# Optimization experiments

Measured on AMD Instinct MI355X. Metric: run time of the kernel, lower is better.

## Reference

```python
import jax, jax.numpy as jnp
import numpy as np


def setup_inputs() -> dict:
    key = jax.random.key(0)
    kq, kk, kv = jax.random.split(key, 3)
    B, L, S, H, E = 2, 2048, 2048, 16, 64
    queries = jax.random.normal(kq, (B, L, H, E), dtype=jnp.float32)
    keys = jax.random.normal(kk, (B, S, H, E), dtype=jnp.float32)
    values = jax.random.normal(kv, (B, S, H, E), dtype=jnp.float32)
    # TriangularCausalMask: True strictly above the diagonal (positions to mask)
    causal = jnp.triu(jnp.ones((L, S), dtype=jnp.bool_), k=1)
    attn_mask = jnp.broadcast_to(causal[None, None, :, :], (B, 1, L, S))
    return {"queries": queries, "keys": keys, "values": values, "attn_mask": attn_mask}


def reference(queries, keys, values, attn_mask):
    # queries: [B,L,H,E], keys/values: [B,S,H,E], attn_mask: [B,1,L,S] bool
    E = queries.shape[-1]
    scale = 1.0 / jnp.sqrt(jnp.asarray(E, dtype=queries.dtype))
    scores = jnp.einsum('blhe,bshe->bhls', queries, keys)      # [B,H,L,S]
    scores = jnp.where(attn_mask, -jnp.inf, scores)
    A = jax.nn.softmax(scale * scores, axis=-1)                # dropout is identity in eval
    V = jnp.einsum('bhls,bshd->blhd', A, values)               # [B,L,H,D]
    return V, A
```

## Files before the change

kernel.cpp:

```cpp
#include <hip/hip_runtime.h>
#include <hip/hip_bf16.h>


#define B_ 2
#define L_ 2048
#define S_ 2048
#define H_ 16
#define E_ 64
#define HE 1024
#define KP 72
#define PP 68

typedef __attribute__((ext_vector_type(8))) __bf16 bfrag;
typedef __attribute__((ext_vector_type(4))) float f32x4;

__device__ __forceinline__ unsigned short f2bu(float x) {
    __bf16 b = (__bf16)x;
    return __builtin_bit_cast(unsigned short, b);
}

__global__ __launch_bounds__(256, 2)
void fullattn_kernel(const float* __restrict__ Qg,
                     const float* __restrict__ Kg,
                     const float* __restrict__ Vg,
                     float* __restrict__ Vout,
                     float* __restrict__ Aout)
{
    __shared__ __align__(16) __bf16 Ks[64 * KP];
    __shared__ __align__(16) __bf16 Vt[64 * KP];
    __shared__ __align__(16) float  Pw[4][16 * PP];

    const int tid  = threadIdx.x;
    const int wave = tid >> 6;
    const int lane = tid & 63;
    const int ln   = lane & 15;
    const int quad = lane >> 4;
    const int lq   = quad * 4;

    const int qt = blockIdx.x;
    const int bh = blockIdx.y;
    const int b  = bh >> 4;
    const int h  = bh & 15;

    const int q0  = qt * 64;
    const int q0w = q0 + wave * 16;

    const float* qbase = Qg + ((size_t)b * L_ * H_ + h) * E_;
    const float* kbase = Kg + ((size_t)b * S_ * H_ + h) * E_;
    const float* vbase = Vg + ((size_t)b * S_ * H_ + h) * E_;
    float* arow0 = Aout + (size_t)bh * L_ * S_;

    bfrag qf[2];
    {
        const float* qr = qbase + (size_t)(q0w + ln) * HE;
        #pragma unroll
        for (int kc = 0; kc < 2; ++kc) {
            const float* p = qr + kc * 32 + quad * 8;
            float4 a0 = *(const float4*)(p);
            float4 a1 = *(const float4*)(p + 4);
            bfrag f;
            f[0] = (__bf16)(a0.x * 0.125f); f[1] = (__bf16)(a0.y * 0.125f);
            f[2] = (__bf16)(a0.z * 0.125f); f[3] = (__bf16)(a0.w * 0.125f);
            f[4] = (__bf16)(a1.x * 0.125f); f[5] = (__bf16)(a1.y * 0.125f);
            f[6] = (__bf16)(a1.z * 0.125f); f[7] = (__bf16)(a1.w * 0.125f);
            qf[kc] = f;
        }
    }

    const int r  = tid >> 2;
    const int c0 = tid & 3;

    float lsum[4] = {0.f, 0.f, 0.f, 0.f};
    for (int st = 0; st <= qt; ++st) {
        const int s0 = st * 64;
        __syncthreads();
        {
            const float* kr = kbase + (size_t)(s0 + r) * HE;
            #pragma unroll
            for (int i = 0; i < 4; ++i) {
                int f4 = c0 + i * 4;
                float4 kv = *(const float4*)(kr + f4 * 4);
                ushort4 kb;
                kb.x = f2bu(kv.x); kb.y = f2bu(kv.y);
                kb.z = f2bu(kv.z); kb.w = f2bu(kv.w);
                *(ushort4*)&Ks[r * KP + f4 * 4] = kb;
            }
        }
        __syncthreads();
        #pragma unroll
        for (int nc = 0; nc < 4; ++nc) {
            f32x4 acc = {0.f, 0.f, 0.f, 0.f};
            #pragma unroll
            for (int kc = 0; kc < 2; ++kc) {
                bfrag bk = *(const bfrag*)&Ks[(nc * 16 + ln) * KP + kc * 32 + quad * 8];
                acc = __builtin_amdgcn_mfma_f32_16x16x32_bf16(qf[kc], bk, acc, 0, 0, 0);
            }
            const int s_abs = s0 + nc * 16 + ln;
            #pragma unroll
            for (int rg = 0; rg < 4; ++rg) {
                const int q_abs = q0w + lq + rg;
                float e = (s_abs <= q_abs) ? __expf(acc[rg]) : 0.0f;
                lsum[rg] += e;
            }
        }
    }

    float inv_l[4];
    #pragma unroll
    for (int rg = 0; rg < 4; ++rg) {
        float v = lsum[rg];
        v += __shfl_xor(v, 1);
        v += __shfl_xor(v, 2);
        v += __shfl_xor(v, 4);
        v += __shfl_xor(v, 8);
        inv_l[rg] = 1.0f / v;
    }

    f32x4 oacc[4];
    #pragma unroll
    for (int dc = 0; dc < 4; ++dc) {
        f32x4 z = {0.f, 0.f, 0.f, 0.f};
        oacc[dc] = z;
    }

    const int wr = lane >> 2;
    const int wc = (lane & 3) * 4;

    for (int st = 0; st <= qt; ++st) {
        const int s0 = st * 64;
        __syncthreads();
        {
            const float* kr = kbase + (size_t)(s0 + r) * HE;
            const float* vr = vbase + (size_t)(s0 + r) * HE;
            #pragma unroll
            for (int i = 0; i < 4; ++i) {
                int f4 = c0 + i * 4;
                float4 kv = *(const float4*)(kr + f4 * 4);
                float4 vv = *(const float4*)(vr + f4 * 4);
                ushort4 kb;
                kb.x = f2bu(kv.x); kb.y = f2bu(kv.y);
                kb.z = f2bu(kv.z); kb.w = f2bu(kv.w);
                *(ushort4*)&Ks[r * KP + f4 * 4] = kb;
                const int d0 = f4 * 4;
                Vt[(d0 + 0) * KP + r] = (__bf16)vv.x;
                Vt[(d0 + 1) * KP + r] = (__bf16)vv.y;
                Vt[(d0 + 2) * KP + r] = (__bf16)vv.z;
                Vt[(d0 + 3) * KP + r] = (__bf16)vv.w;
            }
        }
        __syncthreads();

        #pragma unroll
        for (int nc = 0; nc < 4; ++nc) {
            f32x4 acc = {0.f, 0.f, 0.f, 0.f};
            #pragma unroll
            for (int kc = 0; kc < 2; ++kc) {
                bfrag bk = *(const bfrag*)&Ks[(nc * 16 + ln) * KP + kc * 32 + quad * 8];
                acc = __builtin_amdgcn_mfma_f32_16x16x32_bf16(qf[kc], bk, acc, 0, 0, 0);
            }
            const int s_abs = s0 + nc * 16 + ln;
            #pragma unroll
            for (int rg = 0; rg < 4; ++rg) {
                const int q_abs = q0w + lq + rg;
                float e = (s_abs <= q_abs) ? __expf(acc[rg]) : 0.0f;
                Pw[wave][(lq + rg) * PP + nc * 16 + ln] = e * inv_l[rg];
            }
        }

        bfrag af[2];
        #pragma unroll
        for (int kc = 0; kc < 2; ++kc) {
            const float* pp = &Pw[wave][ln * PP + kc * 32 + quad * 8];
            float4 p0 = *(const float4*)pp;
            float4 p1 = *(const float4*)(pp + 4);
            bfrag f;
            f[0] = (__bf16)p0.x; f[1] = (__bf16)p0.y;
            f[2] = (__bf16)p0.z; f[3] = (__bf16)p0.w;
            f[4] = (__bf16)p1.x; f[5] = (__bf16)p1.y;
            f[6] = (__bf16)p1.z; f[7] = (__bf16)p1.w;
            af[kc] = f;
        }

        #pragma unroll
        for (int dc = 0; dc < 4; ++dc) {
            #pragma unroll
            for (int kc = 0; kc < 2; ++kc) {
                bfrag bv = *(const bfrag*)&Vt[(dc * 16 + ln) * KP + kc * 32 + quad * 8];
                oacc[dc] = __builtin_amdgcn_mfma_f32_16x16x32_bf16(af[kc], bv, oacc[dc], 0, 0, 0);
            }
        }

        float* ar = arow0 + (size_t)(q0w + wr) * S_ + s0;
        #pragma unroll
        for (int c4 = 0; c4 < 4; ++c4) {
            float4 v4 = *(const float4*)&Pw[wave][wr * PP + wc + c4 * 16];
            *(float4*)(ar + wc + c4 * 16) = v4;
        }
    }

    {
        const float4 z4 = {0.f, 0.f, 0.f, 0.f};
        for (int st = qt + 1; st < S_ / 64; ++st) {
            float* ar = arow0 + (size_t)(q0w + wr) * S_ + st * 64;
            #pragma unroll
            for (int c4 = 0; c4 < 4; ++c4)
                *(float4*)(ar + wc + c4 * 16) = z4;
        }
    }

    #pragma unroll
    for (int rg = 0; rg < 4; ++rg) {
        float* vr = Vout + ((size_t)(b * L_ + q0w + lq + rg) * H_ + h) * E_;
        #pragma unroll
        for (int dc = 0; dc < 4; ++dc)
            vr[dc * 16 + ln] = oacc[dc][rg];
    }
}

extern "C" void kernel_launch(void* const* d_in, const int* in_sizes, int n_in,
                              void* d_out, int out_size, void* d_ws, size_t ws_size,
                              hipStream_t stream) {
    const float* Q = (const float*)d_in[0];
    const float* K = (const float*)d_in[1];
    const float* V = (const float*)d_in[2];
    float* out  = (float*)d_out;
    float* Vo   = out;
    float* Ao   = out + (size_t)B_ * L_ * H_ * E_;
    dim3 grid(L_ / 64, B_ * H_);
    fullattn_kernel<<<grid, 256, 0, stream>>>(Q, K, V, Vo, Ao);
}
```

Baseline: 728.7 us.

## Prefetch K/V tiles into registers, balance causal tiles, raise occupancy, set MFMA priority

Loads the next K (and V) tile into registers while the current tile is converted and consumed, so global-load latency overlaps with compute. Block-to-query-tile mapping is interleaved so short and long causal rows are paired, which evens out the load across CUs. Launch bounds are raised to 4 blocks per CU and s_setprio is set around the MFMA sections. The risks are extra register pressure from the prefetch buffers under the tighter occupancy bound, and possible spills.

After: 725.8 us. About the same (-0.4%).

```diff
diff --git a/kernel.cpp b/kernel.cpp
--- a/kernel.cpp
+++ b/kernel.cpp
@@ -19,7 +19,7 @@
     return __builtin_bit_cast(unsigned short, b);
 }
 
-__global__ __launch_bounds__(256, 2)
+__global__ __launch_bounds__(256, 4)
 void fullattn_kernel(const float* __restrict__ Qg,
                      const float* __restrict__ Kg,
                      const float* __restrict__ Vg,
@@ -37,7 +37,8 @@
     const int quad = lane >> 4;
     const int lq   = quad * 4;
 
-    const int qt = blockIdx.x;
+    const int bx = blockIdx.x;
+    const int qt = (bx & 1) ? (31 - (bx >> 1)) : (bx >> 1);
     const int bh = blockIdx.y;
     const int b  = bh >> 4;
     const int h  = bh & 15;
@@ -71,37 +72,60 @@
     const int c0 = tid & 3;
 
     float lsum[4] = {0.f, 0.f, 0.f, 0.f};
+
+    float4 kpre[4];
+    {
+        const float* kr = kbase + (size_t)r * HE;
+        #pragma unroll
+        for (int i = 0; i < 4; ++i)
+            kpre[i] = *(const float4*)(kr + (c0 + i * 4) * 4);
+    }
+
     for (int st = 0; st <= qt; ++st) {
-        const int s0 = st * 64;
-        __syncthreads();
-        {
-            const float* kr = kbase + (size_t)(s0 + r) * HE;
-            #pragma unroll
-            for (int i = 0; i < 4; ++i) {
-                int f4 = c0 + i * 4;
-                float4 kv = *(const float4*)(kr + f4 * 4);
-                ushort4 kb;
-                kb.x = f2bu(kv.x); kb.y = f2bu(kv.y);
-                kb.z = f2bu(kv.z); kb.w = f2bu(kv.w);
-                *(ushort4*)&Ks[r * KP + f4 * 4] = kb;
-            }
+        __syncthreads();
+        #pragma unroll
+        for (int i = 0; i < 4; ++i) {
+            int f4 = c0 + i * 4;
+            ushort4 kb;
+            kb.x = f2bu(kpre[i].x); kb.y = f2bu(kpre[i].y);
+            kb.z = f2bu(kpre[i].z); kb.w = f2bu(kpre[i].w);
+            *(ushort4*)&Ks[r * KP + f4 * 4] = kb;
+        }
+        if (st < qt) {
+            const float* kr = kbase + (size_t)((st + 1) * 64 + r) * HE;
+            #pragma unroll
+            for (int i = 0; i < 4; ++i)
+                kpre[i] = *(const float4*)(kr + (c0 + i * 4) * 4);
         }
         __syncthreads();
         #pragma unroll
         for (int nc = 0; nc < 4; ++nc) {
             f32x4 acc = {0.f, 0.f, 0.f, 0.f};
+            __builtin_amdgcn_s_setprio(1);
             #pragma unroll
             for (int kc = 0; kc < 2; ++kc) {
                 bfrag bk = *(const bfrag*)&Ks[(nc * 16 + ln) * KP + kc * 32 + quad * 8];
                 acc = __builtin_amdgcn_mfma_f32_16x16x32_bf16(qf[kc], bk, acc, 0, 0, 0);
             }
-            const int s_abs = s0 + nc * 16 + ln;
+            __builtin_amdgcn_s_setprio(0);
+            const int s_abs = st * 64 + nc * 16 + ln;
             #pragma unroll
             for (int rg = 0; rg < 4; ++rg) {
                 const int q_abs = q0w + lq + rg;
                 float e = (s_abs <= q_abs) ? __expf(acc[rg]) : 0.0f;
                 lsum[rg] += e;
             }
+        }
+    }
+
+    float4 kp2[4], vp2[4];
+    {
+        const float* kr = kbase + (size_t)r * HE;
+        const float* vr = vbase + (size_t)r * HE;
+        #pragma unroll
+        for (int i = 0; i < 4; ++i) {
+            kp2[i] = *(const float4*)(kr + (c0 + i * 4) * 4);
+            vp2[i] = *(const float4*)(vr + (c0 + i * 4) * 4);
         }
     }
 
@@ -127,25 +151,27 @@
     const int wc = (lane & 3) * 4;
 
     for (int st = 0; st <= qt; ++st) {
-        const int s0 = st * 64;
-        __syncthreads();
-        {
-            const float* kr = kbase + (size_t)(s0 + r) * HE;
-            const float* vr = vbase + (size_t)(s0 + r) * HE;
+        __syncthreads();
+        #pragma unroll
+        for (int i = 0; i < 4; ++i) {
+            int f4 = c0 + i * 4;
+            ushort4 kb;
+            kb.x = f2bu(kp2[i].x); kb.y = f2bu(kp2[i].y);
+            kb.z = f2bu(kp2[i].z); kb.w = f2bu(kp2[i].w);
+            *(ushort4*)&Ks[r * KP + f4 * 4] = kb;
+            const int d0 = f4 * 4;
+            Vt[(d0 + 0) * KP + r] = (__bf16)vp2[i].x;
+            Vt[(d0 + 1) * KP + r] = (__bf16)vp2[i].y;
+            Vt[(d0 + 2) * KP + r] = (__bf16)vp2[i].z;
+            Vt[(d0 + 3) * KP + r] = (__bf16)vp2[i].w;
+        }
+        if (st < qt) {
+            const float* kr = kbase + (size_t)((st + 1) * 64 + r) * HE;
+            const float* vr = vbase + (size_t)((st + 1) * 64 + r) * HE;
             #pragma unroll
             for (int i = 0; i < 4; ++i) {
-                int f4 = c0 + i * 4;
-                float4 kv = *(const float4*)(kr + f4 * 4);
-                float4 vv = *(const float4*)(vr + f4 * 4);
-                ushort4 kb;
-                kb.x = f2bu(kv.x); kb.y = f2bu(kv.y);
-                kb.z = f2bu(kv.z); kb.w = f2bu(kv.w);
-                *(ushort4*)&Ks[r * KP + f4 * 4] = kb;
-                const int d0 = f4 * 4;
-                Vt[(d0 + 0) * KP + r] = (__bf16)vv.x;
-                Vt[(d0 + 1) * KP + r] = (__bf16)vv.y;
-                Vt[(d0 + 2) * KP + r] = (__bf16)vv.z;
-                Vt[(d0 + 3) * KP + r] = (__bf16)vv.w;
+                kp2[i] = *(const float4*)(kr + (c0 + i * 4) * 4);
+                vp2[i] = *(const float4*)(vr + (c0 + i * 4) * 4);
             }
         }
         __syncthreads();
@@ -153,12 +179,14 @@
         #pragma unroll
         for (int nc = 0; nc < 4; ++nc) {
             f32x4 acc = {0.f, 0.f, 0.f, 0.f};
+            __builtin_amdgcn_s_setprio(1);
             #pragma unroll
             for (int kc = 0; kc < 2; ++kc) {
                 bfrag bk = *(const bfrag*)&Ks[(nc * 16 + ln) * KP + kc * 32 + quad * 8];
                 acc = __builtin_amdgcn_mfma_f32_16x16x32_bf16(qf[kc], bk, acc, 0, 0, 0);
             }
-            const int s_abs = s0 + nc * 16 + ln;
+            __builtin_amdgcn_s_setprio(0);
+            const int s_abs = st * 64 + nc * 16 + ln;
             #pragma unroll
             for (int rg = 0; rg < 4; ++rg) {
                 const int q_abs = q0w + lq + rg;
@@ -183,14 +211,16 @@
 
         #pragma unroll
         for (int dc = 0; dc < 4; ++dc) {
+            __builtin_amdgcn_s_setprio(1);
             #pragma unroll
             for (int kc = 0; kc < 2; ++kc) {
                 bfrag bv = *(const bfrag*)&Vt[(dc * 16 + ln) * KP + kc * 32 + quad * 8];
                 oacc[dc] = __builtin_amdgcn_mfma_f32_16x16x32_bf16(af[kc], bv, oacc[dc], 0, 0, 0);
             }
-        }
-
-        float* ar = arow0 + (size_t)(q0w + wr) * S_ + s0;
+            __builtin_amdgcn_s_setprio(0);
+        }
+
+        float* ar = arow0 + (size_t)(q0w + wr) * S_ + st * 64;
         #pragma unroll
         for (int c4 = 0; c4 < 4; ++c4) {
             float4 v4 = *(const float4*)&Pw[wave][wr * PP + wc + c4 * 16];
```

## Precompute bf16 K and transposed V, balance causal work across waves

Applied to the files above, without the earlier changes.

Adds a prep kernel that converts K to bf16 and writes V transposed in bf16 into the workspace. The attention kernel then reads MFMA fragments straight from global memory, with no shared-memory staging or block barriers. Each wave now handles its own 16-row query tile, paired so that each block mixes short and long causal rows (j, 63-j, 64+j, 127-j), and block indices are remapped across heads. The aim is to remove the per-block causal load imbalance and the repeated conversion of K and V. The cost is an extra kernel launch, extra workspace traffic, and loss of LDS reuse of K/V across the waves in a block.

Result: slower. 788.4 us (+8.2%).

```diff
diff --git a/kernel.cpp b/kernel.cpp
--- a/kernel.cpp
+++ b/kernel.cpp
@@ -19,16 +19,52 @@
     return __builtin_bit_cast(unsigned short, b);
 }
 
-__global__ __launch_bounds__(256, 2)
-void fullattn_kernel(const float* __restrict__ Qg,
-                     const float* __restrict__ Kg,
-                     const float* __restrict__ Vg,
-                     float* __restrict__ Vout,
-                     float* __restrict__ Aout)
+__global__ __launch_bounds__(256, 4)
+void prep_kernel(const float* __restrict__ Kg, const float* __restrict__ Vg,
+                 __bf16* __restrict__ Kb, __bf16* __restrict__ Vt)
 {
-    __shared__ __align__(16) __bf16 Ks[64 * KP];
-    __shared__ __align__(16) __bf16 Vt[64 * KP];
-    __shared__ __align__(16) float  Pw[4][16 * PP];
+    __shared__ __align__(16) __bf16 tr[64 * KP];
+    const int t  = threadIdx.x;
+    const int s0 = blockIdx.x * 64;
+    const int bh = blockIdx.y;
+    const int b  = bh >> 4, h = bh & 15;
+    const float* kb_ = Kg + ((size_t)b * S_ * H_ + h) * E_;
+    const float* vb_ = Vg + ((size_t)b * S_ * H_ + h) * E_;
+    const int r = t >> 2, c0 = t & 3;
+    #pragma unroll
+    for (int i = 0; i < 4; ++i) {
+        const int f4 = c0 + i * 4;
+        float4 kv = *(const float4*)(kb_ + (size_t)(s0 + r) * HE + f4 * 4);
+        ushort4 u;
+        u.x = f2bu(kv.x); u.y = f2bu(kv.y); u.z = f2bu(kv.z); u.w = f2bu(kv.w);
+        *(ushort4*)&Kb[((size_t)bh * S_ + s0 + r) * E_ + f4 * 4] = u;
+        float4 vv = *(const float4*)(vb_ + (size_t)(s0 + r) * HE + f4 * 4);
+        const int d0 = f4 * 4;
+        tr[(d0 + 0) * KP + r] = (__bf16)vv.x;
+        tr[(d0 + 1) * KP + r] = (__bf16)vv.y;
+        tr[(d0 + 2) * KP + r] = (__bf16)vv.z;
+        tr[(d0 + 3) * KP + r] = (__bf16)vv.w;
+    }
+    __syncthreads();
+    const int d = t >> 2, sc = t & 3;
+    uint4 w0 = *(const uint4*)&tr[d * KP + sc * 16];
+    uint4 w1 = *(const uint4*)&tr[d * KP + sc * 16 + 8];
+    __bf16* dst = Vt + ((size_t)bh * E_ + d) * S_ + s0 + sc * 16;
+    *(uint4*)(dst)     = w0;
+    *(uint4*)(dst + 8) = w1;
+}
+
+template<bool WS>
+__global__ __launch_bounds__(256, 4)
+void fullattn_wave(const float* __restrict__ Qg,
+                   const float* __restrict__ Kg,
+                   const float* __restrict__ Vg,
+                   const __bf16* __restrict__ Kb,
+                   const __bf16* __restrict__ Vt,
+                   float* __restrict__ Vout,
+                   float* __restrict__ Aout)
+{
+    __shared__ __align__(16) float Pw[4][16 * PP];
 
     const int tid  = threadIdx.x;
     const int wave = tid >> 6;
@@ -37,27 +73,36 @@
     const int quad = lane >> 4;
     const int lq   = quad * 4;
 
-    const int qt = blockIdx.x;
-    const int bh = blockIdx.y;
-    const int b  = bh >> 4;
-    const int h  = bh & 15;
-
-    const int q0  = qt * 64;
-    const int q0w = q0 + wave * 16;
-
-    const float* qbase = Qg + ((size_t)b * L_ * H_ + h) * E_;
-    const float* kbase = Kg + ((size_t)b * S_ * H_ + h) * E_;
-    const float* vbase = Vg + ((size_t)b * S_ * H_ + h) * E_;
+    const int lin = blockIdx.x + 32 * blockIdx.y;
+    const int bh  = ((lin & 7) << 2) | ((lin >> 3) & 3);
+    const int j   = lin >> 5;
+    const int b   = bh >> 4, h = bh & 15;
+
+    int qsel;
+    switch (wave) {
+        case 0:  qsel = j;        break;
+        case 1:  qsel = 63 - j;   break;
+        case 2:  qsel = 64 + j;   break;
+        default: qsel = 127 - j;  break;
+    }
+    const int q0 = qsel * 16;
+    const int nt = ((q0 + 15) >> 6) + 1;
+
+    const float*  qbase = Qg + ((size_t)b * L_ * H_ + h) * E_;
+    const float*  kbase = Kg + ((size_t)b * S_ * H_ + h) * E_;
+    const float*  vbase = Vg + ((size_t)b * S_ * H_ + h) * E_;
+    const __bf16* kbb   = WS ? (Kb + (size_t)bh * S_ * E_) : nullptr;
+    const __bf16* vtb   = WS ? (Vt + (size_t)bh * E_ * S_) : nullptr;
     float* arow0 = Aout + (size_t)bh * L_ * S_;
 
     bfrag qf[2];
     {
-        const float* qr = qbase + (size_t)(q0w + ln) * HE;
+        const float* qr = qbase + (size_t)(q0 + ln) * HE;
         #pragma unroll
         for (int kc = 0; kc < 2; ++kc) {
-            const float* p = qr + kc * 32 + quad * 8;
-            float4 a0 = *(const float4*)(p);
-            float4 a1 = *(const float4*)(p + 4);
+            const float* pq = qr + kc * 32 + quad * 8;
+            float4 a0 = *(const float4*)(pq);
+            float4 a1 = *(const float4*)(pq + 4);
             bfrag f;
             f[0] = (__bf16)(a0.x * 0.125f); f[1] = (__bf16)(a0.y * 0.125f);
             f[2] = (__bf16)(a0.z * 0.125f); f[3] = (__bf16)(a0.w * 0.125f);
@@ -67,38 +112,31 @@
         }
     }
 
-    const int r  = tid >> 2;
-    const int c0 = tid & 3;
-
     float lsum[4] = {0.f, 0.f, 0.f, 0.f};
-    for (int st = 0; st <= qt; ++st) {
-        const int s0 = st * 64;
-        __syncthreads();
-        {
-            const float* kr = kbase + (size_t)(s0 + r) * HE;
-            #pragma unroll
-            for (int i = 0; i < 4; ++i) {
-                int f4 = c0 + i * 4;
-                float4 kv = *(const float4*)(kr + f4 * 4);
-                ushort4 kb;
-                kb.x = f2bu(kv.x); kb.y = f2bu(kv.y);
-                kb.z = f2bu(kv.z); kb.w = f2bu(kv.w);
-                *(ushort4*)&Ks[r * KP + f4 * 4] = kb;
-            }
-        }
-        __syncthreads();
+    for (int st = 0; st < nt; ++st) {
         #pragma unroll
         for (int nc = 0; nc < 4; ++nc) {
             f32x4 acc = {0.f, 0.f, 0.f, 0.f};
             #pragma unroll
             for (int kc = 0; kc < 2; ++kc) {
-                bfrag bk = *(const bfrag*)&Ks[(nc * 16 + ln) * KP + kc * 32 + quad * 8];
+                bfrag bk;
+                if (WS) {
+                    bk = *(const bfrag*)&kbb[(size_t)(st * 64 + nc * 16 + ln) * E_ + kc * 32 + quad * 8];
+                } else {
+                    const float* kp = kbase + (size_t)(st * 64 + nc * 16 + ln) * HE + kc * 32 + quad * 8;
+                    float4 a0 = *(const float4*)(kp);
+                    float4 a1 = *(const float4*)(kp + 4);
+                    bk[0] = (__bf16)a0.x; bk[1] = (__bf16)a0.y;
+                    bk[2] = (__bf16)a0.z; bk[3] = (__bf16)a0.w;
+                    bk[4] = (__bf16)a1.x; bk[5] = (__bf16)a1.y;
+                    bk[6] = (__bf16)a1.z; bk[7] = (__bf16)a1.w;
+                }
                 acc = __builtin_amdgcn_mfma_f32_16x16x32_bf16(qf[kc], bk, acc, 0, 0, 0);
             }
-            const int s_abs = s0 + nc * 16 + ln;
+            const int s_abs = st * 64 + nc * 16 + ln;
             #pragma unroll
             for (int rg = 0; rg < 4; ++rg) {
-                const int q_abs = q0w + lq + rg;
+                const int q_abs = q0 + lq + rg;
                 float e = (s_abs <= q_abs) ? __expf(acc[rg]) : 0.0f;
                 lsum[rg] += e;
             }
@@ -126,47 +164,34 @@
     const int wr = lane >> 2;
     const int wc = (lane & 3) * 4;
 
-    for (int st = 0; st <= qt; ++st) {
-        const int s0 = st * 64;
-        __syncthreads();
-        {
-            const float* kr = kbase + (size_t)(s0 + r) * HE;
-            const float* vr = vbase + (size_t)(s0 + r) * HE;
-            #pragma unroll
-            for (int i = 0; i < 4; ++i) {
-                int f4 = c0 + i * 4;
-                float4 kv = *(const float4*)(kr + f4 * 4);
-                float4 vv = *(const float4*)(vr + f4 * 4);
-                ushort4 kb;
-                kb.x = f2bu(kv.x); kb.y = f2bu(kv.y);
-                kb.z = f2bu(kv.z); kb.w = f2bu(kv.w);
-                *(ushort4*)&Ks[r * KP + f4 * 4] = kb;
-                const int d0 = f4 * 4;
-                Vt[(d0 + 0) * KP + r] = (__bf16)vv.x;
-                Vt[(d0 + 1) * KP + r] = (__bf16)vv.y;
-                Vt[(d0 + 2) * KP + r] = (__bf16)vv.z;
-                Vt[(d0 + 3) * KP + r] = (__bf16)vv.w;
-            }
-        }
-        __syncthreads();
-
+    for (int st = 0; st < nt; ++st) {
         #pragma unroll
         for (int nc = 0; nc < 4; ++nc) {
             f32x4 acc = {0.f, 0.f, 0.f, 0.f};
             #pragma unroll
             for (int kc = 0; kc < 2; ++kc) {
-                bfrag bk = *(const bfrag*)&Ks[(nc * 16 + ln) * KP + kc * 32 + quad * 8];
+                bfrag bk;
+                if (WS) {
+                    bk = *(const bfrag*)&kbb[(size_t)(st * 64 + nc * 16 + ln) * E_ + kc * 32 + quad * 8];
+                } else {
+                    const float* kp = kbase + (size_t)(st * 64 + nc * 16 + ln) * HE + kc * 32 + quad * 8;
+                    float4 a0 = *(const float4*)(kp);
+                    float4 a1 = *(const float4*)(kp + 4);
+                    bk[0] = (__bf16)a0.x; bk[1] = (__bf16)a0.y;
+                    bk[2] = (__bf16)a0.z; bk[3] = (__bf16)a0.w;
+                    bk[4] = (__bf16)a1.x; bk[5] = (__bf16)a1.y;
+                    bk[6] = (__bf16)a1.z; bk[7] = (__bf16)a1.w;
+                }
                 acc = __builtin_amdgcn_mfma_f32_16x16x32_bf16(qf[kc], bk, acc, 0, 0, 0);
             }
-            const int s_abs = s0 + nc * 16 + ln;
+            const int s_abs = st * 64 + nc * 16 + ln;
             #pragma unroll
             for (int rg = 0; rg < 4; ++rg) {
-                const int q_abs = q0w + lq + rg;
+                const int q_abs = q0 + lq + rg;
                 float e = (s_abs <= q_abs) ? __expf(acc[rg]) : 0.0f;
                 Pw[wave][(lq + rg) * PP + nc * 16 + ln] = e * inv_l[rg];
             }
         }
-
         bfrag af[2];
         #pragma unroll
         for (int kc = 0; kc < 2; ++kc) {
@@ -185,12 +210,19 @@
         for (int dc = 0; dc < 4; ++dc) {
             #pragma unroll
             for (int kc = 0; kc < 2; ++kc) {
-                bfrag bv = *(const bfrag*)&Vt[(dc * 16 + ln) * KP + kc * 32 + quad * 8];
+                bfrag bv;
+                if (WS) {
+                    bv = *(const bfrag*)&vtb[(size_t)(dc * 16 + ln) * S_ + st * 64 + kc * 32 + quad * 8];
+                } else {
+                    #pragma unroll
+                    for (int jj = 0; jj < 8; ++jj)
+                        bv[jj] = (__bf16)vbase[(size_t)(st * 64 + kc * 32 + quad * 8 + jj) * HE + dc * 16 + ln];
+                }
                 oacc[dc] = __builtin_amdgcn_mfma_f32_16x16x32_bf16(af[kc], bv, oacc[dc], 0, 0, 0);
             }
         }
 
-        float* ar = arow0 + (size_t)(q0w + wr) * S_ + s0;
+        float* ar = arow0 + (size_t)(q0 + wr) * S_ + st * 64;
         #pragma unroll
         for (int c4 = 0; c4 < 4; ++c4) {
             float4 v4 = *(const float4*)&Pw[wave][wr * PP + wc + c4 * 16];
@@ -200,17 +232,18 @@
 
     {
         const float4 z4 = {0.f, 0.f, 0.f, 0.f};
-        for (int st = qt + 1; st < S_ / 64; ++st) {
-            float* ar = arow0 + (size_t)(q0w + wr) * S_ + st * 64;
-            #pragma unroll
-            for (int c4 = 0; c4 < 4; ++c4)
-                *(float4*)(ar + wc + c4 * 16) = z4;
+        const int z0 = nt * 64;
+        #pragma unroll
+        for (int rg = 0; rg < 4; ++rg) {
+            float* ar = arow0 + (size_t)(q0 + lq + rg) * S_;
+            for (int col = z0 + ln * 4; col < S_; col += 64)
+                *(float4*)(ar + col) = z4;
         }
     }
 
     #pragma unroll
     for (int rg = 0; rg < 4; ++rg) {
-        float* vr = Vout + ((size_t)(b * L_ + q0w + lq + rg) * H_ + h) * E_;
+        float* vr = Vout + ((size_t)(b * L_ + q0 + lq + rg) * H_ + h) * E_;
         #pragma unroll
         for (int dc = 0; dc < 4; ++dc)
             vr[dc * 16 + ln] = oacc[dc][rg];
@@ -223,9 +256,20 @@
     const float* Q = (const float*)d_in[0];
     const float* K = (const float*)d_in[1];
     const float* V = (const float*)d_in[2];
-    float* out  = (float*)d_out;
-    float* Vo   = out;
-    float* Ao   = out + (size_t)B_ * L_ * H_ * E_;
-    dim3 grid(L_ / 64, B_ * H_);
-    fullattn_kernel<<<grid, 256, 0, stream>>>(Q, K, V, Vo, Ao);
-}
+    float* out = (float*)d_out;
+    float* Vo  = out;
+    float* Ao  = out + (size_t)B_ * L_ * H_ * E_;
+
+    const size_t KB_BYTES = (size_t)32 * S_ * E_ * sizeof(__bf16);
+    const bool ws_ok = (d_ws != nullptr) && (ws_size >= 2 * KB_BYTES);
+    __bf16* Kb = (__bf16*)d_ws;
+    __bf16* Vt = (__bf16*)((char*)d_ws + KB_BYTES);
+
+    dim3 grid(32, 32);
+    if (ws_ok) {
+        prep_kernel<<<grid, 256, 0, stream>>>(K, V, Kb, Vt);
+        fullattn_wave<true><<<grid, 256, 0, stream>>>(Q, K, V, Kb, Vt, Vo, Ao);
+    } else {
+        fullattn_wave<false><<<grid, 256, 0, stream>>>(Q, K, V, nullptr, nullptr, Vo, Ao);
+    }
+}
```
